# Optimization experiments

Measured on AMD Instinct MI355X. Metric: run time of the kernel, lower is better.

## Reference

```python
import jax, jax.numpy as jnp
import numpy as np

C_GMS = 0.0026  # constant c in the GMS map


def _median3(x):
    # 3x3 median with zero padding (matches kornia MedianBlur: conv2d-unfold
    # with zero padding, then median of the 9 values; odd count so torch's
    # lower-median == true median). x: [B,1,H,W]
    B, C, H, W = x.shape
    xp = jnp.pad(x, ((0, 0), (0, 0), (1, 1), (1, 1)))
    patches = jnp.stack(
        [xp[:, :, i:i + H, j:j + W] for i in range(3) for j in range(3)], axis=0
    )  # [9,B,1,H,W]
    return jnp.median(patches, axis=0)


def _prewitt(x):
    # fixed 2-channel Prewitt conv, VALID padding, then gradient magnitude
    Gx = jnp.array([[-1., 0., 1.], [-1., 0., 1.], [-1., 0., 1.]], dtype=x.dtype) / 3.0
    Gy = jnp.array([[1., 1., 1.], [0., 0., 0.], [-1., -1., -1.]], dtype=x.dtype) / 3.0
    k = jnp.stack([Gx, Gy])[:, None]  # [2,1,3,3] OIHW
    g = jax.lax.conv_general_dilated(
        x, k, window_strides=(1, 1), padding='VALID',
        dimension_numbers=('NCHW', 'OIHW', 'NCHW'))  # [B,2,H-2,W-2]
    return jnp.sqrt(jnp.sum(g * g, axis=1, keepdims=True))


def _gms_loss(Ii, Ir):
    x = jnp.mean(Ii, axis=1, keepdims=True)  # channel mean -> grayscale
    y = jnp.mean(Ir, axis=1, keepdims=True)
    gI = _prewitt(_median3(x))
    gR = _prewitt(_median3(y))
    gmap = (2.0 * gI * gR + C_GMS) / (gI * gI + gR * gR + C_GMS)
    return jnp.mean(1.0 - gmap)


def _avg_pool2(x):
    # avg_pool2d(kernel=2, stride=2)
    B, C, H, W = x.shape
    return x.reshape(B, C, H // 2, 2, W // 2, 2).mean(axis=(3, 5))


def setup_inputs() -> dict:
    key = jax.random.key(0)
    k1, k2 = jax.random.split(key)
    Ii = jax.random.uniform(k1, (16, 3, 512, 512), dtype=jnp.float32)
    Ir = jax.random.uniform(k2, (16, 3, 512, 512), dtype=jnp.float32)
    return {"Ii": Ii, "Ir": Ir}


def reference(Ii, Ir):
    total = _gms_loss(Ii, Ir)
    for _ in range(3):  # fixed 4-scale pyramid
        Ii = _avg_pool2(Ii)
        Ir = _avg_pool2(Ir)
        total = total + _gms_loss(Ii, Ir)
    return total / 4.0
```

## Files before the change

### kernel.cpp

```cpp
#include <hip/hip_runtime.h>

#define C_GMS 0.0026f

__device__ __forceinline__ float dppL(float x) {
    return __int_as_float(__builtin_amdgcn_mov_dpp(__float_as_int(x), 0x138, 0xf, 0xf, true));
}
__device__ __forceinline__ float dppR(float x) {
    return __int_as_float(__builtin_amdgcn_mov_dpp(__float_as_int(x), 0x130, 0xf, 0xf, true));
}
__device__ __forceinline__ float med3f(float a, float b, float c) {
    return __builtin_amdgcn_fmed3f(a, b, c);
}

#define N0 4608
#define N1 2560
#define N2 768
#define N3 256
#define NTOT 8192

template<int TRIP, class LoadFn, class PoolFn>
__device__ __forceinline__ float gms_core(int lane, int Hk, int R0, int iend, int c,
                                          int phalf, LoadFn loadrow2, PoolFn dopool)
{
    auto medrow = [&](float ga, float gb, float gc, float& m, float& rs) {
        float lo = fminf(fminf(ga, gb), gc);
        float me = med3f(ga, gb, gc);
        float hi = fmaxf(fmaxf(ga, gb), gc);
        float lmax = fmaxf(fmaxf(dppL(lo), lo), dppR(lo));
        float mid  = med3f(dppL(me), me, dppR(me));
        float hmin = fminf(fminf(dppL(hi), hi), dppR(hi));
        m  = med3f(lmax, mid, hmin);
        rs = m + dppL(m) + dppR(m);
    };

    float xa, ya, xb, yb, xc, yc, xd, yd, xe, ye;
    loadrow2(R0 - 1, xa, ya);
    loadrow2(R0,     xb, yb);
    loadrow2(R0 + 1, xc, yc);
    loadrow2(R0 + 2, xd, yd);
    loadrow2(R0 + 3, xe, ye);

    float n0x, n0y, n1x, n1y;
    loadrow2(R0 + 4, n0x, n0y);
    loadrow2(R0 + 5, n1x, n1y);

    float mx0, mx1, mx2, rx0, rx1, rx2;
    float my0, my1, my2, ry0, ry1, ry2;
    medrow(xa, xb, xc, mx0, rx0); medrow(ya, yb, yc, my0, ry0);
    dopool(xb, xc, yb, yc, phalf);
    medrow(xb, xc, xd, mx1, rx1); medrow(yb, yc, yd, my1, ry1);
    medrow(xc, xd, xe, mx2, rx2); medrow(yc, yd, ye, my2, ry2);

    float gx2 = xd, gx3 = xe, gy2 = yd, gy3 = ye;
    const bool outLane = (lane >= 2) && (lane <= 61) && (c <= Hk - 2);
    const float C9 = 9.0f * C_GMS;
    float acc = 0.0f;

    #pragma unroll
    for (int j = 0; j < TRIP; ++j) {
        const int i = R0 + j;
        float pfx, pfy;
        loadrow2(i + 6, pfx, pfy);

        float csx = mx0 + mx1 + mx2;
        float csy = my0 + my1 + my2;
        float Gxx = dppR(csx) - dppL(csx);
        float Gxy = dppR(csy) - dppL(csy);
        float Gyx = rx0 - rx2;
        float Gyy = ry0 - ry2;
        float a = fmaf(Gxx, Gxx, Gyx * Gyx);
        float b = fmaf(Gxy, Gxy, Gyy * Gyy);
        float t = a + b;
        float s = __builtin_amdgcn_sqrtf(a * b);
        float den = t + C9;
        float diff = fmaf(-2.0f, s, t);
        float r = __builtin_amdgcn_rcpf(den);
        if (outLane && (i < iend)) acc = fmaf(diff, r, acc);

        if (((i + 3) & 1) == 1) dopool(gx2, gx3, gy2, gy3, (i + 2) >> 1);

        float mxn, rxn, myn, ryn;
        medrow(gx2, gx3, n0x, mxn, rxn);
        medrow(gy2, gy3, n0y, myn, ryn);
        mx0 = mx1; mx1 = mx2; mx2 = mxn; rx0 = rx1; rx1 = rx2; rx2 = rxn;
        my0 = my1; my1 = my2; my2 = myn; ry0 = ry1; ry1 = ry2; ry2 = ryn;
        gx2 = gx3; gx3 = n0x; gy2 = gy3; gy3 = n0y;
        n0x = n1x; n0y = n1y; n1x = pfx; n1y = pfy;
    }

    for (int off = 32; off; off >>= 1) acc += __shfl_down(acc, off, 64);
    return acc;
}

__global__ __launch_bounds__(256) void msgms_scale0(
    const float* __restrict__ Ii, const float* __restrict__ Ir,
    float* __restrict__ X1, float* __restrict__ Y1, float* __restrict__ P)
{
    const int lane = threadIdx.x & 63;
    const int u = blockIdx.x * 4 + (threadIdx.x >> 6);
    const int s  = u % 9;
    const int t1 = u / 9;
    const int k  = t1 % 32;
    const int b  = t1 / 32;

    const int c  = 60 * s - 1 + lane;
    const int R0 = k * 16;
    const int iend = min(R0 + 16, 510);

    const float* PX = Ii + (size_t)b * 3 * 262144;
    const float* PY = Ir + (size_t)b * 3 * 262144;

    const int cc = min(max(c, 0), 511);
    const float cw = ((c >= 0) && (c < 512)) ? (1.0f / 3.0f) : 0.0f;

    auto loadrow2 = [&](int r, float& vx, float& vy) {
        int rc = min(max(r, 0), 511);
        float m = (r == rc) ? cw : 0.0f;
        int o = rc * 512 + cc;
        float x0 = PX[o], x1 = PX[o + 262144], x2 = PX[o + 524288];
        float y0 = PY[o], y1 = PY[o + 262144], y2 = PY[o + 524288];
        vx = (x0 + x1 + x2) * m;
        vy = (y0 + y1 + y2) * m;
    };

    const int phalf = R0 >> 1;
    const int pend  = min(phalf + 8, 256);
    const bool poolLane = ((lane & 1) == 1) && (lane <= 59) && (c + 1 < 512);
    auto dopool = [&](float bx, float cx, float by, float cy, int p) {
        if (p < phalf || p >= pend) return;
        float ux = bx + cx, uy = by + cy;
        float hx = ux + dppR(ux);
        float hy = uy + dppR(uy);
        if (poolLane) {
            size_t o = ((size_t)b * 256 + p) * 256 + (c >> 1);
            X1[o] = hx * 0.25f;
            Y1[o] = hy * 0.25f;
        }
    };

    float acc = gms_core<16>(lane, 512, R0, iend, c, phalf, loadrow2, dopool);
    if (lane == 0) P[u] = acc;
}

template<int G>
__device__ __forceinline__ void phaseR(
    int u, const float* __restrict__ X1, const float* __restrict__ Y1,
    int nstrips, int nchunks, float* __restrict__ P)
{
    constexpr int Hk = 256 / G;
    const int lane = threadIdx.x & 63;
    const int s  = u % nstrips;
    const int t1 = u / nstrips;
    const int k  = t1 % nchunks;
    const int b  = t1 / nchunks;

    const int c  = 60 * s - 1 + lane;
    const int R0 = k * 8;
    const int iend = min(R0 + 8, Hk - 2);

    const float* Xp = X1 + (size_t)b * 65536;
    const float* Yp = Y1 + (size_t)b * 65536;

    const int cc = min(max(c, 0), Hk - 1);
    const float cval = ((c >= 0) && (c < Hk)) ? 1.0f : 0.0f;

    auto loadrow2 = [&](int r, float& vx, float& vy) {
        int rc = min(max(r, 0), Hk - 1);
        float m = (r == rc) ? cval : 0.0f;
        if constexpr (G == 1) {
            int o = rc * 256 + cc;
            vx = Xp[o] * m; vy = Yp[o] * m;
        } else if constexpr (G == 2) {
            int o = (rc * 2) * 256 + cc * 2;
            float2 a0 = *(const float2*)(Xp + o);
            float2 a1 = *(const float2*)(Xp + o + 256);
            float2 b0 = *(const float2*)(Yp + o);
            float2 b1 = *(const float2*)(Yp + o + 256);
            float q = 0.25f * m;
            vx = ((a0.x + a0.y) + (a1.x + a1.y)) * q;
            vy = ((b0.x + b0.y) + (b1.x + b1.y)) * q;
        } else {
            int o = (rc * 4) * 256 + cc * 4;
            float sx = 0.0f, sy = 0.0f;
            #pragma unroll
            for (int fr = 0; fr < 4; ++fr) {
                float4 t = *(const float4*)(Xp + o + fr * 256);
                float4 q = *(const float4*)(Yp + o + fr * 256);
                sx += (t.x + t.y) + (t.z + t.w);
                sy += (q.x + q.y) + (q.z + q.w);
            }
            float q = 0.0625f * m;
            vx = sx * q; vy = sy * q;
        }
    };
    auto nopool = [&](float, float, float, float, int) {};

    float acc = gms_core<8>(lane, Hk, R0, iend, c, 0, loadrow2, nopool);
    if (lane == 0) P[u] = acc;
}

__global__ __launch_bounds__(256) void msgms_rest(
    const float* __restrict__ X1, const float* __restrict__ Y1,
    float* __restrict__ P)
{
    const int u = blockIdx.x * 4 + (threadIdx.x >> 6);
    if      (u < N1)      phaseR<1>(u,           X1, Y1, 5, 32, P + N0);
    else if (u < N1 + N2) phaseR<2>(u - N1,      X1, Y1, 3, 16, P + N0 + N1);
    else                  phaseR<4>(u - N1 - N2, X1, Y1, 2,  8, P + N0 + N1 + N2);
}

__global__ __launch_bounds__(256) void msgms_final(
    const float* __restrict__ P, float* __restrict__ out)
{
    const int tid = threadIdx.x;
    const double w0 = 1.0 / (4.0 * 16.0 * 510.0 * 510.0);
    const double w1 = 1.0 / (4.0 * 16.0 * 254.0 * 254.0);
    const double w2 = 1.0 / (4.0 * 16.0 * 126.0 * 126.0);
    const double w3 = 1.0 / (4.0 * 16.0 * 62.0 * 62.0);
    double v = 0.0;
    for (int i = tid; i < NTOT; i += 256) {
        double w = (i < N0) ? w0 : (i < N0 + N1) ? w1 : (i < N0 + N1 + N2) ? w2 : w3;
        v += (double)P[i] * w;
    }
    for (int off = 32; off; off >>= 1) v += __shfl_down(v, off, 64);
    __shared__ double wsum[4];
    if ((tid & 63) == 0) wsum[tid >> 6] = v;
    __syncthreads();
    if (tid == 0) out[0] = (float)(wsum[0] + wsum[1] + wsum[2] + wsum[3]);
}

extern "C" void kernel_launch(void* const* d_in, const int* in_sizes, int n_in,
                              void* d_out, int out_size, void* d_ws, size_t ws_size,
                              hipStream_t stream) {
    const float* Ii = (const float*)d_in[0];
    const float* Ir = (const float*)d_in[1];
    float* out = (float*)d_out;

    char* ws = (char*)d_ws;
    float* P  = (float*)ws;
    float* X1 = P + NTOT;
    float* Y1 = X1 + 16 * 256 * 256;

    msgms_scale0<<<N0 / 4, 256, 0, stream>>>(Ii, Ir, X1, Y1, P);
    msgms_rest<<<(N1 + N2 + N3) / 4, 256, 0, stream>>>(X1, Y1, P);
    msgms_final<<<1, 256, 0, stream>>>(P, out);
}
```

Measured before the change: 140.4 us.

## Process two columns per lane in scale-0 kernel with float2 loads

The scale-0 kernel now has each lane handle two adjacent columns, using float2 loads, and computes the median, Prewitt and pooling steps for both columns in registers. Strips widen from 60 to 120 output columns, which cuts the wave count from 9 to 5 per row chunk. This lowers halo recomputation and doubles the bytes per load instruction. The cost is higher register pressure and more complex boundary logic for output and pooling lanes.

```diff
diff --git a/kernel.cpp b/kernel.cpp
--- a/kernel.cpp
+++ b/kernel.cpp
@@ -12,11 +12,11 @@
     return __builtin_amdgcn_fmed3f(a, b, c);
 }
 
-#define N0 4608
+#define N0 2560
 #define N1 2560
 #define N2 768
 #define N3 256
-#define NTOT 8192
+#define NTOT 6144
 
 template<int TRIP, class LoadFn, class PoolFn>
 __device__ __forceinline__ float gms_core(int lane, int Hk, int R0, int iend, int c,
@@ -98,47 +98,138 @@
 {
     const int lane = threadIdx.x & 63;
     const int u = blockIdx.x * 4 + (threadIdx.x >> 6);
-    const int s  = u % 9;
-    const int t1 = u / 9;
+    const int s  = u % 5;
+    const int t1 = u / 5;
     const int k  = t1 % 32;
     const int b  = t1 / 32;
 
-    const int c  = 60 * s - 1 + lane;
+    const int B  = 120 * s;
+    const int c0 = B + 2 * lane;
     const int R0 = k * 16;
     const int iend = min(R0 + 16, 510);
 
     const float* PX = Ii + (size_t)b * 3 * 262144;
     const float* PY = Ir + (size_t)b * 3 * 262144;
 
-    const int cc = min(max(c, 0), 511);
-    const float cw = ((c >= 0) && (c < 512)) ? (1.0f / 3.0f) : 0.0f;
-
-    auto loadrow2 = [&](int r, float& vx, float& vy) {
+    const int cc = min(c0, 510);
+    const float cw = (c0 <= 511) ? (1.0f / 3.0f) : 0.0f;
+
+    auto loadrow2 = [&](int r, float2& vx, float2& vy) {
         int rc = min(max(r, 0), 511);
         float m = (r == rc) ? cw : 0.0f;
         int o = rc * 512 + cc;
-        float x0 = PX[o], x1 = PX[o + 262144], x2 = PX[o + 524288];
-        float y0 = PY[o], y1 = PY[o + 262144], y2 = PY[o + 524288];
-        vx = (x0 + x1 + x2) * m;
-        vy = (y0 + y1 + y2) * m;
-    };
-
+        float2 x0 = *(const float2*)(PX + o);
+        float2 x1 = *(const float2*)(PX + o + 262144);
+        float2 x2 = *(const float2*)(PX + o + 524288);
+        float2 y0 = *(const float2*)(PY + o);
+        float2 y1 = *(const float2*)(PY + o + 262144);
+        float2 y2 = *(const float2*)(PY + o + 524288);
+        vx.x = (x0.x + x1.x + x2.x) * m; vx.y = (x0.y + x1.y + x2.y) * m;
+        vy.x = (y0.x + y1.x + y2.x) * m; vy.y = (y0.y + y1.y + y2.y) * m;
+    };
+
+    auto medrow = [&](float2 ga, float2 gb, float2 gc, float2& m, float2& rs) {
+        float lo0 = fminf(fminf(ga.x, gb.x), gc.x);
+        float lo1 = fminf(fminf(ga.y, gb.y), gc.y);
+        float me0 = med3f(ga.x, gb.x, gc.x);
+        float me1 = med3f(ga.y, gb.y, gc.y);
+        float hi0 = fmaxf(fmaxf(ga.x, gb.x), gc.x);
+        float hi1 = fmaxf(fmaxf(ga.y, gb.y), gc.y);
+        float lmax0 = fmaxf(fmaxf(dppL(lo1), lo0), lo1);
+        float lmax1 = fmaxf(fmaxf(lo0, lo1), dppR(lo0));
+        float mid0  = med3f(dppL(me1), me0, me1);
+        float mid1  = med3f(me0, me1, dppR(me0));
+        float hmin0 = fminf(fminf(dppL(hi1), hi0), hi1);
+        float hmin1 = fminf(fminf(hi0, hi1), dppR(hi0));
+        m.x = med3f(lmax0, mid0, hmin0);
+        m.y = med3f(lmax1, mid1, hmin1);
+        float ms = m.x + m.y;
+        rs.x = dppL(m.y) + ms;
+        rs.y = ms + dppR(m.x);
+    };
+
+    const int ostart = (s == 0) ? 1 : (120 * s + 6);
+    const int oend   = (s == 4) ? 510 : (120 * s + 125);
+    const bool out0 = (c0 >= ostart)     && (c0 <= oend);
+    const bool out1 = (c0 + 1 >= ostart) && (c0 + 1 <= oend);
+
+    const int q = 60 * s + lane;
+    const bool poolLane = (lane < ((s == 4) ? 16 : 60));
     const int phalf = R0 >> 1;
     const int pend  = min(phalf + 8, 256);
-    const bool poolLane = ((lane & 1) == 1) && (lane <= 59) && (c + 1 < 512);
-    auto dopool = [&](float bx, float cx, float by, float cy, int p) {
+    auto dopool = [&](float2 bx, float2 cx, float2 by, float2 cy, int p) {
         if (p < phalf || p >= pend) return;
-        float ux = bx + cx, uy = by + cy;
-        float hx = ux + dppR(ux);
-        float hy = uy + dppR(uy);
         if (poolLane) {
-            size_t o = ((size_t)b * 256 + p) * 256 + (c >> 1);
-            X1[o] = hx * 0.25f;
-            Y1[o] = hy * 0.25f;
+            size_t o = ((size_t)b * 256 + p) * 256 + q;
+            X1[o] = ((bx.x + bx.y) + (cx.x + cx.y)) * 0.25f;
+            Y1[o] = ((by.x + by.y) + (cy.x + cy.y)) * 0.25f;
         }
     };
 
-    float acc = gms_core<16>(lane, 512, R0, iend, c, phalf, loadrow2, dopool);
+    float2 xa, ya, xb, yb, xc, yc, xd, yd, xe, ye;
+    loadrow2(R0 - 1, xa, ya);
+    loadrow2(R0,     xb, yb);
+    loadrow2(R0 + 1, xc, yc);
+    loadrow2(R0 + 2, xd, yd);
+    loadrow2(R0 + 3, xe, ye);
+
+    float2 n0x, n0y, n1x, n1y;
+    loadrow2(R0 + 4, n0x, n0y);
+    loadrow2(R0 + 5, n1x, n1y);
+
+    float2 mx0, mx1, mx2, rx0, rx1, rx2;
+    float2 my0, my1, my2, ry0, ry1, ry2;
+    medrow(xa, xb, xc, mx0, rx0); medrow(ya, yb, yc, my0, ry0);
+    dopool(xb, xc, yb, yc, phalf);
+    medrow(xb, xc, xd, mx1, rx1); medrow(yb, yc, yd, my1, ry1);
+    medrow(xc, xd, xe, mx2, rx2); medrow(yc, yd, ye, my2, ry2);
+
+    float2 gx2 = xd, gx3 = xe, gy2 = yd, gy3 = ye;
+    const float C9 = 9.0f * C_GMS;
+    float acc = 0.0f;
+
+    #pragma unroll
+    for (int j = 0; j < 16; ++j) {
+        const int i = R0 + j;
+        float2 pfx, pfy;
+        loadrow2(i + 6, pfx, pfy);
+
+        float2 csx, csy;
+        csx.x = mx0.x + mx1.x + mx2.x; csx.y = mx0.y + mx1.y + mx2.y;
+        csy.x = my0.x + my1.x + my2.x; csy.y = my0.y + my1.y + my2.y;
+        float Gxx0 = csx.y - dppL(csx.y), Gxx1 = dppR(csx.x) - csx.x;
+        float Gxy0 = csy.y - dppL(csy.y), Gxy1 = dppR(csy.x) - csy.x;
+        float Gyx0 = rx0.x - rx2.x,       Gyx1 = rx0.y - rx2.y;
+        float Gyy0 = ry0.x - ry2.x,       Gyy1 = ry0.y - ry2.y;
+
+        float a0 = fmaf(Gxx0, Gxx0, Gyx0 * Gyx0);
+        float b0 = fmaf(Gxy0, Gxy0, Gyy0 * Gyy0);
+        float t0 = a0 + b0;
+        float s0 = __builtin_amdgcn_sqrtf(a0 * b0);
+        float d0 = fmaf(-2.0f, s0, t0);
+        float r0 = __builtin_amdgcn_rcpf(t0 + C9);
+        if (out0 && (i < iend)) acc = fmaf(d0, r0, acc);
+
+        float a1 = fmaf(Gxx1, Gxx1, Gyx1 * Gyx1);
+        float b1 = fmaf(Gxy1, Gxy1, Gyy1 * Gyy1);
+        float t1v = a1 + b1;
+        float s1 = __builtin_amdgcn_sqrtf(a1 * b1);
+        float d1 = fmaf(-2.0f, s1, t1v);
+        float r1 = __builtin_amdgcn_rcpf(t1v + C9);
+        if (out1 && (i < iend)) acc = fmaf(d1, r1, acc);
+
+        if (((i + 3) & 1) == 1) dopool(gx2, gx3, gy2, gy3, (i + 2) >> 1);
+
+        float2 mxn, rxn, myn, ryn;
+        medrow(gx2, gx3, n0x, mxn, rxn);
+        medrow(gy2, gy3, n0y, myn, ryn);
+        mx0 = mx1; mx1 = mx2; mx2 = mxn; rx0 = rx1; rx1 = rx2; rx2 = rxn;
+        my0 = my1; my1 = my2; my2 = myn; ry0 = ry1; ry1 = ry2; ry2 = ryn;
+        gx2 = gx3; gx3 = n0x; gy2 = gy3; gy3 = n0y;
+        n0x = n1x; n0y = n1y; n1x = pfx; n1y = pfy;
+    }
+
+    for (int off = 32; off; off >>= 1) acc += __shfl_down(acc, off, 64);
     if (lane == 0) P[u] = acc;
 }
 
```

New measurement: 144.5 us. 3.0% more time.
